# Optimization experiments

Hardware: AMD Instinct MI355X
Metric: run time of the kernel (lower is better)

Reference implementation:

```python
import jax, jax.numpy as jnp
import numpy as np


def setup_inputs() -> dict:
    key = jax.random.key(0)
    ks = jax.random.split(key, 4)
    B, T, D, U = 64, 2048, 256, 256
    x = jax.random.normal(ks[0], (B, T, D), dtype=jnp.float32)
    s = 1.0 / np.sqrt(D)
    kz = jax.random.normal(ks[1], (D, U), dtype=jnp.float32) * s
    kr = jax.random.normal(ks[2], (D, U), dtype=jnp.float32) * s
    kh = jax.random.normal(ks[3], (D, U), dtype=jnp.float32) * s
    return {
        'x': x, 'kz': kz, 'kr': kr, 'kh': kh,
        'mz': jnp.ones((U,), jnp.float32), 'mr': jnp.ones((U,), jnp.float32),
        'bz': jnp.zeros((U,), jnp.float32), 'br': jnp.zeros((U,), jnp.float32),
        'bh': jnp.zeros((U,), jnp.float32),
    }


def reference(x, kz, kr, kh, mz, mr, bz, br, bh):
    # Precompute the three input projections for all timesteps (batched GEMMs),
    # then scan the purely elementwise recurrence over time.
    xz = jnp.einsum('btd,du->btu', x, kz) + bz  # [B,T,U]
    xr = jnp.einsum('btd,du->btu', x, kr) + br
    xh = jnp.einsum('btd,du->btu', x, kh) + bh
    B, T, U = xz.shape
    h0 = jnp.zeros((B, U), x.dtype)

    def step(h, inp):
        xz_t, xr_t, xh_t = inp
        r = jnp.tanh(xr_t + h * mr) + 1.0
        z = jax.nn.sigmoid(xz_t + h * mz)
        hh = jnp.tanh(xh_t + r * h)
        out = (1.0 - z) * hh + z * h
        return out, out

    # scan over time axis: move T to leading axis
    xs = (jnp.swapaxes(xz, 0, 1), jnp.swapaxes(xr, 0, 1), jnp.swapaxes(xh, 0, 1))
    _, ys = jax.lax.scan(step, h0, xs)
    return jnp.swapaxes(ys, 0, 1)  # [B,T,U]
```

## Files before the change

kernel.cpp:

```cpp
#include <hip/hip_runtime.h>
#include <hip/hip_bf16.h>

#define BB 64
#define TT 2048
#define DD 256
#define UU 256
#define MM (BB*TT)
#define NN (3*UU)
#define PLANE ((size_t)BB*TT*UU)

typedef _Float16 half8 __attribute__((ext_vector_type(8)));
typedef _Float16 half4 __attribute__((ext_vector_type(4)));
typedef float floatx4 __attribute__((ext_vector_type(4)));

__device__ inline float fexp2(float x){
#if __has_builtin(__builtin_amdgcn_exp2f)
  return __builtin_amdgcn_exp2f(x);
#else
  return exp2f(x);
#endif
}
__device__ inline float frcp(float x){
#if __has_builtin(__builtin_amdgcn_rcpf)
  return __builtin_amdgcn_rcpf(x);
#else
  return 1.0f/x;
#endif
}
__device__ inline float ftanh(float a){
  const float TWO_L2E = 2.8853900817779268f;
  return 1.0f - 2.0f*frcp(fexp2(TWO_L2E*a) + 1.0f);
}
__device__ inline float fsigmoid(float a){
  const float L2E = 1.4426950408889634f;
  return frcp(1.0f + fexp2(-L2E*a));
}

__global__ __launch_bounds__(256) void prep_kernel(const float* __restrict__ kz,
                                                   const float* __restrict__ kr,
                                                   const float* __restrict__ kh,
                                                   _Float16* __restrict__ K16T){
  int o = blockIdx.x*256 + threadIdx.x;
  int n = o >> 8;
  int k = o & 255;
  int p = n >> 8;
  int u = n & 255;
  const float* w = (p==0) ? kz : ((p==1) ? kr : kh);
  K16T[o] = (_Float16)w[k*UU + u];
}

#define BM 128
#define BN 128
#define BK 32
#define LDA 40

__global__ __launch_bounds__(256) void gemm_kernel(const float* __restrict__ X,
                                                   const _Float16* __restrict__ K16T,
                                                   const float* __restrict__ bz,
                                                   const float* __restrict__ br,
                                                   const float* __restrict__ bh,
                                                   _Float16* __restrict__ P){
  __shared__ __align__(16) _Float16 As[BM*LDA];
  __shared__ __align__(16) _Float16 Bs[BN*BK];
  const int tid = threadIdx.x;
  const int bx = blockIdx.x;
  const int by = blockIdx.y;
  const int rowBase = by*BM;
  const int nBase = bx*BN;

  const int wave = tid >> 6, lane = tid & 63;
  const int wm = wave & 1, wn = wave >> 1;
  const int lrow = lane & 15, lkq = lane >> 4;

  floatx4 acc[4][4] = {};

  const int arow = tid >> 1;
  const int acol = (tid & 1) * 16;
  const float* aptr = X + (size_t)(rowBase + arow)*DD + acol;
  _Float16* asdst = &As[arow*LDA + acol];

  for (int k0 = 0; k0 < DD; k0 += BK) {
    __syncthreads();
    #pragma unroll
    for (int i = 0; i < 2; i++) {
      int c = i*256 + tid;
      const _Float16* g = K16T + (size_t)(nBase + (c>>2))*DD + k0 + (c&3)*8;
      __builtin_amdgcn_global_load_lds(
          (const __attribute__((address_space(1))) void*)g,
          (__attribute__((address_space(3))) void*)(Bs + c*8),
          16, 0, 0);
    }
    floatx4 a0 = *(const floatx4*)(aptr + k0);
    floatx4 a1 = *(const floatx4*)(aptr + k0 + 4);
    floatx4 a2 = *(const floatx4*)(aptr + k0 + 8);
    floatx4 a3 = *(const floatx4*)(aptr + k0 + 12);
    half8 pk0, pk1;
    #pragma unroll
    for (int q = 0; q < 4; q++){
      pk0[q]   = (_Float16)a0[q];
      pk0[4+q] = (_Float16)a1[q];
      pk1[q]   = (_Float16)a2[q];
      pk1[4+q] = (_Float16)a3[q];
    }
    *(half8*)asdst       = pk0;
    *(half8*)(asdst + 8) = pk1;
    __syncthreads();
    half8 af[4], bf[4];
    #pragma unroll
    for (int i = 0; i < 4; i++)
      af[i] = *(const half8*)&As[(wm*64 + i*16 + lrow)*LDA + lkq*8];
    #pragma unroll
    for (int j = 0; j < 4; j++)
      bf[j] = *(const half8*)&Bs[(wn*64 + j*16 + lrow)*BK + lkq*8];
    #pragma unroll
    for (int i = 0; i < 4; i++)
      #pragma unroll
      for (int j = 0; j < 4; j++)
        acc[i][j] = __builtin_amdgcn_mfma_f32_16x16x32_f16(af[i], bf[j], acc[i][j], 0, 0, 0);
  }

  const int p = bx >> 1;
  const int ub = (bx & 1) * 128;
  const float* bias = (p==0) ? bz : ((p==1) ? br : bh);
  _Float16* Pp = P + (size_t)p * PLANE;
  const int bidx = rowBase >> 11;
  const int t0 = (rowBase & 2047) + wm*64 + lkq*4;
  #pragma unroll
  for (int j = 0; j < 4; j++){
    int col = ub + wn*64 + j*16 + lrow;
    float bv = bias[col];
    _Float16* rowp = Pp + (size_t)(bidx*UU + col)*TT + t0;
    #pragma unroll
    for (int i = 0; i < 4; i++){
      half4 v;
      #pragma unroll
      for (int r = 0; r < 4; r++)
        v[r] = (_Float16)(acc[i][j][r] + bv);
      *(half4*)(rowp + i*16) = v;
    }
  }
}

#define PF 16
#define NBUF 4
__global__ __launch_bounds__(64) void scan_kernel(const _Float16* __restrict__ P,
                                                  const float* __restrict__ mz,
                                                  const float* __restrict__ mr,
                                                  float* __restrict__ out){
  const int ci = blockIdx.x*64 + threadIdx.x;
  const int b = ci >> 8;
  const int u = ci & 255;
  const half8* pz = (const half8*)(P + (size_t)ci*TT);
  const half8* pr = (const half8*)(P + PLANE + (size_t)ci*TT);
  const half8* ph = (const half8*)(P + 2*PLANE + (size_t)ci*TT);
  float* po = out + (size_t)b*(TT*UU) + u;
  const float vmz = mz[u], vmr = mr[u];
  float h = 0.0f;

  half8 qz[NBUF][2], qr[NBUF][2], qh[NBUF][2];

#define LOADC(buf, c) do { \
    qz[buf][0] = pz[(c)*2];   qz[buf][1] = pz[(c)*2+1]; \
    qr[buf][0] = pr[(c)*2];   qr[buf][1] = pr[(c)*2+1]; \
    qh[buf][0] = ph[(c)*2];   qh[buf][1] = ph[(c)*2+1]; \
  } while(0)

#define PROC(buf, c) do { \
    _Pragma("unroll") \
    for (int i = 0; i < PF; i++){ \
      float xz = (float)qz[buf][i>>3][i&7]; \
      float xr = (float)qr[buf][i>>3][i&7]; \
      float xh = (float)qh[buf][i>>3][i&7]; \
      float r  = ftanh(xr + h*vmr) + 1.0f; \
      float z  = fsigmoid(xz + h*vmz); \
      float hh = ftanh(xh + r*h); \
      h = (1.0f - z)*hh + z*h; \
      po[(size_t)((c)*PF + i)*UU] = h; \
    } \
    if ((c) + NBUF < NC) LOADC(buf, (c) + NBUF); \
  } while(0)

  const int NC = TT/PF;
  LOADC(0, 0); LOADC(1, 1); LOADC(2, 2); LOADC(3, 3);
  for (int c = 0; c < NC; c += NBUF){
    PROC(0, c);
    PROC(1, c+1);
    PROC(2, c+2);
    PROC(3, c+3);
  }
#undef LOADC
#undef PROC
}

extern "C" void kernel_launch(void* const* d_in, const int* in_sizes, int n_in,
                              void* d_out, int out_size, void* d_ws, size_t ws_size,
                              hipStream_t stream) {
  (void)in_sizes; (void)n_in; (void)out_size; (void)ws_size;
  const float* x  = (const float*)d_in[0];
  const float* kz = (const float*)d_in[1];
  const float* kr = (const float*)d_in[2];
  const float* kh = (const float*)d_in[3];
  const float* mz = (const float*)d_in[4];
  const float* mr = (const float*)d_in[5];
  const float* bz = (const float*)d_in[6];
  const float* br = (const float*)d_in[7];
  const float* bh = (const float*)d_in[8];
  float* out = (float*)d_out;

  _Float16* K16T = (_Float16*)d_ws;
  _Float16* P    = (_Float16*)((char*)d_ws + 393216);

  hipLaunchKernelGGL(prep_kernel, dim3(NN*DD/256), dim3(256), 0, stream, kz, kr, kh, K16T);
  hipLaunchKernelGGL(gemm_kernel, dim3(NN/BN, MM/BM), dim3(256), 0, stream,
                     x, K16T, bz, br, bh, P);
  hipLaunchKernelGGL(scan_kernel, dim3(256), dim3(64), 0, stream, P, mz, mr, out);
}
```

Before: 467.1 us.

## Double-buffer GEMM LDS tiles and remap blocks across XCDs

Adds a two-stage LDS ping-pong in the projection GEMM: the next K-slice of weights and activations is issued before the current slice's MFMAs, and the staged activations are written to the other buffer afterwards, so each K step needs one barrier instead of two. It also remaps the linear block id so that all six N-tiles of a row panel land on the same XCD, improving L2 reuse of the X rows. This costs double the LDS and more live registers, which may lower occupancy. The scan kernel, which likely dominates total time, is unchanged.

```diff
diff --git a/kernel.cpp b/kernel.cpp
--- a/kernel.cpp
+++ b/kernel.cpp
@@ -60,13 +60,18 @@
                                                    const float* __restrict__ br,
                                                    const float* __restrict__ bh,
                                                    _Float16* __restrict__ P){
-  __shared__ __align__(16) _Float16 As[BM*LDA];
-  __shared__ __align__(16) _Float16 Bs[BN*BK];
+  __shared__ __align__(16) _Float16 As[2][BM*LDA];
+  __shared__ __align__(16) _Float16 Bs[2][BN*BK];
   const int tid = threadIdx.x;
-  const int bx = blockIdx.x;
-  const int by = blockIdx.y;
+
+  const int l   = blockIdx.y*6 + blockIdx.x;
+  const int xcd = l & 7;
+  const int idx = l >> 3;
+  const int pnl = idx / 6;
+  const int by  = xcd*128 + pnl;
+  const int bx  = idx - pnl*6;
   const int rowBase = by*BM;
-  const int nBase = bx*BN;
+  const int nBase   = bx*BN;
 
   const int wave = tid >> 6, lane = tid & 63;
   const int wm = wave & 1, wn = wave >> 1;
@@ -77,23 +82,22 @@
   const int arow = tid >> 1;
   const int acol = (tid & 1) * 16;
   const float* aptr = X + (size_t)(rowBase + arow)*DD + acol;
-  _Float16* asdst = &As[arow*LDA + acol];
-
-  for (int k0 = 0; k0 < DD; k0 += BK) {
-    __syncthreads();
-    #pragma unroll
-    for (int i = 0; i < 2; i++) {
-      int c = i*256 + tid;
-      const _Float16* g = K16T + (size_t)(nBase + (c>>2))*DD + k0 + (c&3)*8;
-      __builtin_amdgcn_global_load_lds(
-          (const __attribute__((address_space(1))) void*)g,
-          (__attribute__((address_space(3))) void*)(Bs + c*8),
-          16, 0, 0);
-    }
-    floatx4 a0 = *(const floatx4*)(aptr + k0);
-    floatx4 a1 = *(const floatx4*)(aptr + k0 + 4);
-    floatx4 a2 = *(const floatx4*)(aptr + k0 + 8);
-    floatx4 a3 = *(const floatx4*)(aptr + k0 + 12);
+
+  const int c0 = tid, c1 = 256 + tid;
+  const _Float16* bsrc0 = K16T + (size_t)(nBase + (c0>>2))*DD + (c0&3)*8;
+  const _Float16* bsrc1 = K16T + (size_t)(nBase + (c1>>2))*DD + (c1&3)*8;
+
+  __builtin_amdgcn_global_load_lds(
+      (const __attribute__((address_space(1))) void*)bsrc0,
+      (__attribute__((address_space(3))) void*)(&Bs[0][c0*8]), 16, 0, 0);
+  __builtin_amdgcn_global_load_lds(
+      (const __attribute__((address_space(1))) void*)bsrc1,
+      (__attribute__((address_space(3))) void*)(&Bs[0][c1*8]), 16, 0, 0);
+  {
+    floatx4 a0 = *(const floatx4*)(aptr);
+    floatx4 a1 = *(const floatx4*)(aptr + 4);
+    floatx4 a2 = *(const floatx4*)(aptr + 8);
+    floatx4 a3 = *(const floatx4*)(aptr + 12);
     half8 pk0, pk1;
     #pragma unroll
     for (int q = 0; q < 4; q++){
@@ -102,21 +106,55 @@
       pk1[q]   = (_Float16)a2[q];
       pk1[4+q] = (_Float16)a3[q];
     }
-    *(half8*)asdst       = pk0;
-    *(half8*)(asdst + 8) = pk1;
-    __syncthreads();
+    _Float16* asd = &As[0][arow*LDA + acol];
+    *(half8*)asd       = pk0;
+    *(half8*)(asd + 8) = pk1;
+  }
+  __syncthreads();
+
+  #pragma unroll
+  for (int kk = 0; kk < 8; kk++){
+    const int cur = kk & 1, nxt = cur ^ 1;
+    floatx4 a0, a1, a2, a3;
+    if (kk < 7){
+      const int k0n = (kk+1)*BK;
+      __builtin_amdgcn_global_load_lds(
+          (const __attribute__((address_space(1))) void*)(bsrc0 + k0n),
+          (__attribute__((address_space(3))) void*)(&Bs[nxt][c0*8]), 16, 0, 0);
+      __builtin_amdgcn_global_load_lds(
+          (const __attribute__((address_space(1))) void*)(bsrc1 + k0n),
+          (__attribute__((address_space(3))) void*)(&Bs[nxt][c1*8]), 16, 0, 0);
+      a0 = *(const floatx4*)(aptr + k0n);
+      a1 = *(const floatx4*)(aptr + k0n + 4);
+      a2 = *(const floatx4*)(aptr + k0n + 8);
+      a3 = *(const floatx4*)(aptr + k0n + 12);
+    }
     half8 af[4], bf[4];
     #pragma unroll
     for (int i = 0; i < 4; i++)
-      af[i] = *(const half8*)&As[(wm*64 + i*16 + lrow)*LDA + lkq*8];
+      af[i] = *(const half8*)&As[cur][(wm*64 + i*16 + lrow)*LDA + lkq*8];
     #pragma unroll
     for (int j = 0; j < 4; j++)
-      bf[j] = *(const half8*)&Bs[(wn*64 + j*16 + lrow)*BK + lkq*8];
+      bf[j] = *(const half8*)&Bs[cur][(wn*64 + j*16 + lrow)*BK + lkq*8];
     #pragma unroll
     for (int i = 0; i < 4; i++)
       #pragma unroll
       for (int j = 0; j < 4; j++)
         acc[i][j] = __builtin_amdgcn_mfma_f32_16x16x32_f16(af[i], bf[j], acc[i][j], 0, 0, 0);
+    if (kk < 7){
+      half8 pk0, pk1;
+      #pragma unroll
+      for (int q = 0; q < 4; q++){
+        pk0[q]   = (_Float16)a0[q];
+        pk0[4+q] = (_Float16)a1[q];
+        pk1[q]   = (_Float16)a2[q];
+        pk1[4+q] = (_Float16)a3[q];
+      }
+      _Float16* asd = &As[nxt][arow*LDA + acol];
+      *(half8*)asd       = pk0;
+      *(half8*)(asd + 8) = pk1;
+    }
+    __syncthreads();
   }
 
   const int p = bx >> 1;
```

Result: slower. 501.8 us (+7.4%).
